# Optimization experiments

Hardware: AMD Instinct MI355X
Metric: run time of the kernel (lower is better)

The kernel has to match this reference:

```python
import jax, jax.numpy as jnp
import numpy as np

B, C, H, W = 256, 512, 14, 14  # C = rnn_size
S = 7                          # spp_size

def setup_inputs() -> dict:
    key = jax.random.key(0)
    ks = jax.random.split(key, 8)
    sd = 1.0 / np.sqrt(C)
    return {
        "att_v": jax.random.normal(ks[0], (B, C, H, W), dtype=jnp.float32),
        "h": jax.random.normal(ks[1], (B, C), dtype=jnp.float32),
        # a2a: Linear(rnn_size, rnn_size)
        "Wa": jax.random.uniform(ks[2], (C, C), jnp.float32, -sd, sd),
        "ba": jax.random.uniform(ks[3], (C,), jnp.float32, -sd, sd),
        # h2a: Linear(rnn_size, rnn_size)
        "Wh": jax.random.uniform(ks[4], (C, C), jnp.float32, -sd, sd),
        "bh": jax.random.uniform(ks[5], (C,), jnp.float32, -sd, sd),
        # d2d: Linear(rnn_size, 1)
        "Wd": jax.random.uniform(ks[6], (C,), jnp.float32, -sd, sd),
        "bd": jax.random.uniform(ks[7], (1,), jnp.float32, -sd, sd),
    }

def reference(att_v, h, Wa, ba, Wh, bh, Wd, bd):
    b, c, hh, ww = att_v.shape
    # AdaptiveAvgPool2d(S) with H,W divisible by S -> block mean
    pooled = att_v.reshape(b, c, S, hh // S, S, ww // S).mean(axis=(3, 5))  # [B,C,S,S]
    a = pooled.reshape(b, c, S * S).transpose(0, 2, 1)  # [B, N=49, C]
    av = jnp.einsum('bnc,dc->bnd', a, Wa) + ba          # a2a, torch Linear: x @ W.T + b
    ah = h @ Wh.T + bh                                  # h2a, [B,C]
    dot = jnp.tanh(av + ah[:, None, :])                 # broadcast add + tanh
    scores = jnp.einsum('bnd,d->bn', dot, Wd) + bd[0]   # d2d -> [B, N]
    weight = jax.nn.softmax(scores, axis=-1)            # over attention positions
    att_res = jnp.einsum('bnc,bn->bc', a, weight)       # bmm(att^T, weight)
    return att_res
```

## Files before the change

kernel.cpp:

```cpp
#include <hip/hip_runtime.h>
#include <hip/hip_bf16.h>

#define BATCH 256
#define CDIM  512
#define NPOS  49
#define MROWS 12544
#define ASTRIDE 520

typedef __attribute__((ext_vector_type(8))) short bf16x8_t;
typedef __attribute__((ext_vector_type(4))) float f32x4_t;

#define WS_NEED 15081472u

__device__ __forceinline__ void load_lds16(const void* g, void* l) {
    __builtin_amdgcn_global_load_lds(
        (const __attribute__((address_space(1))) void*)g,
        (__attribute__((address_space(3))) void*)l, 16, 0, 0);
}

__global__ __launch_bounds__(256) void prep(
    const float* __restrict__ Wa, const float* __restrict__ Wh,
    const float* __restrict__ h,
    __hip_bfloat16* __restrict__ Wab, __hip_bfloat16* __restrict__ Whb,
    __hip_bfloat16* __restrict__ hb) {
    int gid = blockIdx.x * 256 + threadIdx.x;
    const float* src; __hip_bfloat16* dst; int idx;
    if (gid < 65536)       { src = Wa; dst = Wab; idx = gid; }
    else if (gid < 131072) { src = Wh; dst = Whb; idx = gid - 65536; }
    else                   { src = h;  dst = hb;  idx = gid - 131072; }
    float4 v = ((const float4*)src)[idx];
    dst[idx * 4 + 0] = __float2bfloat16(v.x);
    dst[idx * 4 + 1] = __float2bfloat16(v.y);
    dst[idx * 4 + 2] = __float2bfloat16(v.z);
    dst[idx * 4 + 3] = __float2bfloat16(v.w);
}

__global__ __launch_bounds__(256, 6) void pool_kernel(
    const float* __restrict__ att_v, __hip_bfloat16* __restrict__ pooled) {
    __shared__ float4 lds[32 * 49];
    const int b  = blockIdx.x >> 4;
    const int cg = blockIdx.x & 15;
    const int t  = threadIdx.x;

    const float4* src = (const float4*)(att_v + ((size_t)b * CDIM + cg * 32) * 196);
    #pragma unroll
    for (int k = 0; k < 7; ++k) {
        int idx = t + k * 256;
        if (idx < 1568) lds[idx] = src[idx];
    }
    __syncthreads();

    const int i = t >> 5;
    const int c = t & 31;
    if (i < 7) {
        const float4* fp = &lds[c * 49 + 7 * i];
        float4 f0 = fp[0], f1 = fp[1], f2 = fp[2], f3 = fp[3];
        float4 f4 = fp[4], f5 = fp[5], f6 = fp[6];
        float p[7];
        p[0] = f0.x + f0.y + f3.z + f3.w;
        p[1] = f0.z + f0.w + f4.x + f4.y;
        p[2] = f1.x + f1.y + f4.z + f4.w;
        p[3] = f1.z + f1.w + f5.x + f5.y;
        p[4] = f2.x + f2.y + f5.z + f5.w;
        p[5] = f2.z + f2.w + f6.x + f6.y;
        p[6] = f3.x + f3.y + f6.z + f6.w;
        __hip_bfloat16* outp = pooled + ((size_t)b * NPOS + i * 7) * CDIM + cg * 32 + c;
        #pragma unroll
        for (int j = 0; j < 7; ++j)
            outp[(size_t)j * CDIM] = __float2bfloat16(p[j] * 0.25f);
    }
}

__global__ __launch_bounds__(256, 4) void ah_gemm(
    const __hip_bfloat16* __restrict__ A,
    const __hip_bfloat16* __restrict__ Bw,
    const float* __restrict__ ba, const float* __restrict__ bh,
    float* __restrict__ ahb) {
    __shared__ __hip_bfloat16 aT[64 * 32];
    __shared__ __hip_bfloat16 bT[64 * 32];
    const int mt = blockIdx.x & 3;
    const int nt = blockIdx.x >> 2;
    const int t = threadIdx.x;
    const int wave = t >> 6, lane = t & 63;
    const int wm = wave & 1, wn = wave >> 1;
    const int q = lane >> 4, r = lane & 15;
    const int m0 = mt * 64, n0 = nt * 64;

    const __hip_bfloat16* Ag = A + (size_t)(m0 + (t >> 2)) * CDIM + (t & 3) * 8;
    const __hip_bfloat16* Bg = Bw + (size_t)(n0 + (t >> 2)) * CDIM + (t & 3) * 8;
    char* aD = (char*)aT + t * 16;
    char* bD = (char*)bT + t * 16;

    f32x4_t acc[2][2];
    #pragma unroll
    for (int rt = 0; rt < 2; ++rt)
        #pragma unroll
        for (int ct = 0; ct < 2; ++ct) acc[rt][ct] = (f32x4_t){0.f, 0.f, 0.f, 0.f};

    for (int ks = 0; ks < 16; ++ks) {
        load_lds16(Ag + ks * 32, aD);
        load_lds16(Bg + ks * 32, bD);
        __syncthreads();
        bf16x8_t af[2], bf[2];
        #pragma unroll
        for (int rt = 0; rt < 2; ++rt)
            af[rt] = *(const bf16x8_t*)&aT[(wm * 32 + rt * 16 + r) * 32 + q * 8];
        #pragma unroll
        for (int ct = 0; ct < 2; ++ct)
            bf[ct] = *(const bf16x8_t*)&bT[(wn * 32 + ct * 16 + r) * 32 + q * 8];
        #pragma unroll
        for (int rt = 0; rt < 2; ++rt)
            #pragma unroll
            for (int ct = 0; ct < 2; ++ct)
                acc[rt][ct] = __builtin_amdgcn_mfma_f32_16x16x32_bf16(
                    af[rt], bf[ct], acc[rt][ct], 0, 0, 0);
        __syncthreads();
    }
    #pragma unroll
    for (int ct = 0; ct < 2; ++ct) {
        const int col = n0 + wn * 32 + ct * 16 + r;
        const float bias = ba[col] + bh[col];
        #pragma unroll
        for (int rt = 0; rt < 2; ++rt)
            #pragma unroll
            for (int rg = 0; rg < 4; ++rg) {
                const int row = m0 + wm * 32 + rt * 16 + q * 4 + rg;
                ahb[(size_t)row * CDIM + col] = acc[rt][ct][rg] + bias;
            }
    }
}

__global__ __launch_bounds__(256, 4) void gemm_score3(
    const __hip_bfloat16* __restrict__ A,
    const __hip_bfloat16* __restrict__ Bw,
    const float* __restrict__ ahb,
    const float* __restrict__ Wd,
    float* __restrict__ scores8) {
    __shared__ __hip_bfloat16 aT[64 * 32];
    __shared__ __hip_bfloat16 bT[128 * 32];
    const int b  = blockIdx.x >> 2;
    const int nt = blockIdx.x & 3;
    const int t = threadIdx.x;
    const int wave = t >> 6, lane = t & 63;
    const int wm = wave & 1, wn = wave >> 1;
    const int q = lane >> 4, r = lane & 15;
    const int m0 = b * NPOS;
    const int n0 = nt * 128;

    const __hip_bfloat16* Ag = A + (size_t)(m0 + (t >> 2)) * CDIM + (t & 3) * 8;
    const __hip_bfloat16* Bg = Bw + (size_t)(n0 + (t >> 2)) * CDIM + (t & 3) * 8;
    char* aD = (char*)aT + t * 16;
    char* bD = (char*)bT + t * 16;

    f32x4_t acc[2][4];
    #pragma unroll
    for (int rt = 0; rt < 2; ++rt)
        #pragma unroll
        for (int ct = 0; ct < 4; ++ct) acc[rt][ct] = (f32x4_t){0.f, 0.f, 0.f, 0.f};

    for (int ks = 0; ks < 16; ++ks) {
        load_lds16(Ag + ks * 32, aD);
        load_lds16(Bg + ks * 32, bD);
        load_lds16(Bg + (size_t)64 * CDIM + ks * 32, bD + 4096);
        __syncthreads();
        bf16x8_t af[2], bf[4];
        #pragma unroll
        for (int rt = 0; rt < 2; ++rt)
            af[rt] = *(const bf16x8_t*)&aT[(wm * 32 + rt * 16 + r) * 32 + q * 8];
        #pragma unroll
        for (int ct = 0; ct < 4; ++ct)
            bf[ct] = *(const bf16x8_t*)&bT[(wn * 64 + ct * 16 + r) * 32 + q * 8];
        #pragma unroll
        for (int rt = 0; rt < 2; ++rt)
            #pragma unroll
            for (int ct = 0; ct < 4; ++ct)
                acc[rt][ct] = __builtin_amdgcn_mfma_f32_16x16x32_bf16(
                    af[rt], bf[ct], acc[rt][ct], 0, 0, 0);
        __syncthreads();
    }

    float rsum[2][4];
    #pragma unroll
    for (int rt = 0; rt < 2; ++rt)
        #pragma unroll
        for (int rg = 0; rg < 4; ++rg) rsum[rt][rg] = 0.f;

    const float* ahp = ahb + (size_t)b * CDIM;
    #pragma unroll
    for (int ct = 0; ct < 4; ++ct) {
        const int col = n0 + wn * 64 + ct * 16 + r;
        const float ah = ahp[col];
        const float wd = Wd[col];
        #pragma unroll
        for (int rt = 0; rt < 2; ++rt)
            #pragma unroll
            for (int rg = 0; rg < 4; ++rg) {
                float x = acc[rt][ct][rg] + ah;
                float e = __expf(2.f * x);
                rsum[rt][rg] += (1.f - 2.f / (e + 1.f)) * wd;
            }
    }
    #pragma unroll
    for (int m = 1; m < 16; m <<= 1)
        #pragma unroll
        for (int rt = 0; rt < 2; ++rt)
            #pragma unroll
            for (int rg = 0; rg < 4; ++rg)
                rsum[rt][rg] += __shfl_xor(rsum[rt][rg], m, 64);
    if (r == 0) {
        float* seg = scores8 + (size_t)(nt * 2 + wn) * MROWS + m0;
        #pragma unroll
        for (int rt = 0; rt < 2; ++rt)
            #pragma unroll
            for (int rg = 0; rg < 4; ++rg) {
                const int row = wm * 32 + rt * 16 + q * 4 + rg;
                if (row < NPOS) seg[row] = rsum[rt][rg];
            }
    }
}

__global__ __launch_bounds__(256) void softmax_wsum(
    const float* __restrict__ scores8, const __hip_bfloat16* __restrict__ pooled,
    float* __restrict__ out) {
    __shared__ float s_lds[NPOS];
    const int b  = blockIdx.x >> 1;
    const int ch = (blockIdx.x & 1) * 256 + threadIdx.x;
    if (threadIdx.x < NPOS) {
        float s = 0.f;
        #pragma unroll
        for (int seg = 0; seg < 8; ++seg)
            s += scores8[(size_t)seg * MROWS + b * NPOS + threadIdx.x];
        s_lds[threadIdx.x] = s;
    }
    __syncthreads();
    float vmax = -3.0e38f;
    #pragma unroll
    for (int n = 0; n < NPOS; ++n) vmax = fmaxf(vmax, s_lds[n]);
    const __hip_bfloat16* Ap = pooled + (size_t)b * NPOS * CDIM + ch;
    float sum = 0.f, accv = 0.f;
    #pragma unroll
    for (int n = 0; n < NPOS; ++n) {
        float e = __expf(s_lds[n] - vmax);
        sum += e;
        accv += e * __bfloat162float(Ap[(size_t)n * CDIM]);
    }
    out[b * CDIM + ch] = accv / sum;
}

__global__ void prep_convert(const float* __restrict__ Wa,
                             const float* __restrict__ Wh,
                             __hip_bfloat16* __restrict__ Wab,
                             __hip_bfloat16* __restrict__ Whb) {
    int gid = blockIdx.x * blockDim.x + threadIdx.x;
    const int quarter = (CDIM * CDIM) / 4;
    const float4* src; __hip_bfloat16* dst; int idx;
    if (gid < quarter) { src = (const float4*)Wa; dst = Wab; idx = gid; }
    else               { src = (const float4*)Wh; dst = Whb; idx = gid - quarter; }
    float4 v = src[idx];
    dst[idx * 4 + 0] = __float2bfloat16(v.x);
    dst[idx * 4 + 1] = __float2bfloat16(v.y);
    dst[idx * 4 + 2] = __float2bfloat16(v.z);
    dst[idx * 4 + 3] = __float2bfloat16(v.w);
}

__global__ __launch_bounds__(512, 2) void att_spp_main(
    const float* __restrict__ att_v, const float* __restrict__ h,
    const float* __restrict__ ba, const float* __restrict__ bh,
    const float* __restrict__ Wd,
    const __hip_bfloat16* __restrict__ Wab, const __hip_bfloat16* __restrict__ Whb,
    float* __restrict__ out) {
    __shared__ __hip_bfloat16 a_lds[64 * ASTRIDE];
    __shared__ __hip_bfloat16 h_lds[CDIM];
    __shared__ float babh_lds[CDIM];
    __shared__ float wd_lds[CDIM];
    __shared__ float scores_lds[64];
    __shared__ float weights_lds[NPOS];
    const int b = blockIdx.x, t = threadIdx.x;
    h_lds[t]    = __float2bfloat16(h[b * CDIM + t]);
    babh_lds[t] = ba[t] + bh[t];
    wd_lds[t]   = Wd[t];
    if (t < 64) scores_lds[t] = 0.f;
    for (int idx = t; idx < (64 - NPOS) * ASTRIDE; idx += 512)
        a_lds[NPOS * ASTRIDE + idx] = __float2bfloat16(0.f);
    {
        const int jj = t & 7, g = t >> 3;
        const float2* att2 = (const float2*)(att_v + (size_t)b * CDIM * 196);
        if (jj < 7) {
            for (int ci = 0; ci < 8; ++ci) {
                const int c = g + (ci << 6), cbase = c * 98;
                #pragma unroll
                for (int i = 0; i < 7; ++i) {
                    float2 v0 = att2[cbase + i * 14 + jj];
                    float2 v1 = att2[cbase + i * 14 + 7 + jj];
                    a_lds[(i * 7 + jj) * ASTRIDE + c] =
                        __float2bfloat16((v0.x + v0.y + v1.x + v1.y) * 0.25f);
                }
            }
        }
    }
    __syncthreads();
    const int wave = t >> 6, lane = t & 63, q = lane >> 4, r = lane & 15;
    f32x4_t acc[4][4];
    #pragma unroll
    for (int rt = 0; rt < 4; ++rt)
        #pragma unroll
        for (int ct = 0; ct < 4; ++ct) acc[rt][ct] = (f32x4_t){0.f,0.f,0.f,0.f};
    const int dBase = wave * 64 + r;
    for (int ks = 0; ks < 16; ++ks) {
        const int k0 = ks * 32 + q * 8;
        bf16x8_t af[4], bf[4];
        #pragma unroll
        for (int rt = 0; rt < 4; ++rt)
            af[rt] = *(const bf16x8_t*)&a_lds[(rt * 16 + r) * ASTRIDE + k0];
        #pragma unroll
        for (int ct = 0; ct < 4; ++ct)
            bf[ct] = *(const bf16x8_t*)&Wab[(size_t)(dBase + ct * 16) * CDIM + k0];
        #pragma unroll
        for (int rt = 0; rt < 4; ++rt)
            #pragma unroll
            for (int ct = 0; ct < 4; ++ct)
                acc[rt][ct] = __builtin_amdgcn_mfma_f32_16x16x32_bf16(
                    af[rt], bf[ct], acc[rt][ct], 0, 0, 0);
    }
    for (int ks = 0; ks < 16; ++ks) {
        const int k0 = ks * 32 + q * 8;
        bf16x8_t af = *(const bf16x8_t*)&h_lds[k0];
        bf16x8_t bf[4];
        #pragma unroll
        for (int ct = 0; ct < 4; ++ct)
            bf[ct] = *(const bf16x8_t*)&Whb[(size_t)(dBase + ct * 16) * CDIM + k0];
        #pragma unroll
        for (int rt = 0; rt < 4; ++rt)
            #pragma unroll
            for (int ct = 0; ct < 4; ++ct)
                acc[rt][ct] = __builtin_amdgcn_mfma_f32_16x16x32_bf16(
                    af, bf[ct], acc[rt][ct], 0, 0, 0);
    }
    float part[4][4];
    #pragma unroll
    for (int rt = 0; rt < 4; ++rt)
        #pragma unroll
        for (int rg = 0; rg < 4; ++rg) part[rt][rg] = 0.f;
    #pragma unroll
    for (int ct = 0; ct < 4; ++ct) {
        const int d = dBase + ct * 16;
        const float bias = babh_lds[d], wd = wd_lds[d];
        #pragma unroll
        for (int rt = 0; rt < 4; ++rt)
            #pragma unroll
            for (int rg = 0; rg < 4; ++rg) {
                float x = acc[rt][ct][rg] + bias;
                float e = __expf(2.f * x);
                part[rt][rg] += (1.f - 2.f / (e + 1.f)) * wd;
            }
    }
    #pragma unroll
    for (int m = 1; m < 16; m <<= 1)
        #pragma unroll
        for (int rt = 0; rt < 4; ++rt)
            #pragma unroll
            for (int rg = 0; rg < 4; ++rg)
                part[rt][rg] += __shfl_xor(part[rt][rg], m, 64);
    if (r == 0) {
        #pragma unroll
        for (int rt = 0; rt < 4; ++rt)
            #pragma unroll
            for (int rg = 0; rg < 4; ++rg)
                atomicAdd(&scores_lds[rt * 16 + q * 4 + rg], part[rt][rg]);
    }
    __syncthreads();
    if (wave == 0) {
        float v = (lane < NPOS) ? scores_lds[lane] : -3.0e38f;
        float vmax = v;
        #pragma unroll
        for (int m = 1; m < 64; m <<= 1) vmax = fmaxf(vmax, __shfl_xor(vmax, m, 64));
        float e = (lane < NPOS) ? __expf(v - vmax) : 0.f;
        float s = e;
        #pragma unroll
        for (int m = 1; m < 64; m <<= 1) s += __shfl_xor(s, m, 64);
        if (lane < NPOS) weights_lds[lane] = e / s;
    }
    __syncthreads();
    float sum = 0.f;
    #pragma unroll
    for (int n = 0; n < NPOS; ++n)
        sum += __bfloat162float(a_lds[n * ASTRIDE + t]) * weights_lds[n];
    out[b * CDIM + t] = sum;
}

extern "C" void kernel_launch(void* const* d_in, const int* in_sizes, int n_in,
                              void* d_out, int out_size, void* d_ws, size_t ws_size,
                              hipStream_t stream) {
    const float* att_v = (const float*)d_in[0];
    const float* h     = (const float*)d_in[1];
    const float* Wa    = (const float*)d_in[2];
    const float* ba    = (const float*)d_in[3];
    const float* Wh    = (const float*)d_in[4];
    const float* bh    = (const float*)d_in[5];
    const float* Wd    = (const float*)d_in[6];

    if (ws_size >= WS_NEED) {
        char* ws = (char*)d_ws;
        __hip_bfloat16* Wab     = (__hip_bfloat16*)(ws);
        __hip_bfloat16* Whb     = (__hip_bfloat16*)(ws + 524288);
        __hip_bfloat16* hb      = (__hip_bfloat16*)(ws + 1048576);
        __hip_bfloat16* pooled  = (__hip_bfloat16*)(ws + 1310720);
        float*          ahb     = (float*)(ws + 14155776);
        float*          scores8 = (float*)(ws + 14680064);

        prep<<<640, 256, 0, stream>>>(Wa, Wh, h, Wab, Whb, hb);
        pool_kernel<<<4096, 256, 0, stream>>>(att_v, pooled);
        ah_gemm<<<32, 256, 0, stream>>>(hb, Whb, ba, bh, ahb);
        gemm_score3<<<1024, 256, 0, stream>>>(pooled, Wab, ahb, Wd, scores8);
        softmax_wsum<<<512, 256, 0, stream>>>(scores8, pooled, (float*)d_out);
    } else {
        __hip_bfloat16* Wab = (__hip_bfloat16*)d_ws;
        __hip_bfloat16* Whb = Wab + (size_t)CDIM * CDIM;
        prep_convert<<<512, 256, 0, stream>>>(Wa, Wh, Wab, Whb);
        att_spp_main<<<BATCH, 512, 0, stream>>>(att_v, h, ba, bh, Wd, Wab, Whb,
                                                (float*)d_out);
    }
}
```

Baseline: 198.8 us.

## Fuse pool, weight prep and h2a GEMV into one kernel; deepen K step

Merges the prep, pooling and ah_gemm launches into a single kernel whose block ranges handle pooling, Wa bf16 conversion and an fp32 h2a GEMV per batch. This drops two launches and the Wh/h bf16 conversion. The score GEMM now loads 64-wide K slices per barrier, halving the number of sync rounds at the cost of double the LDS. The h2a path becomes a scalar fp32 GEMV with strided Wh row reads, which may be slow and uncoalesced.

```diff
diff --git a/kernel.cpp b/kernel.cpp
--- a/kernel.cpp
+++ b/kernel.cpp
@@ -10,7 +10,7 @@
 typedef __attribute__((ext_vector_type(8))) short bf16x8_t;
 typedef __attribute__((ext_vector_type(4))) float f32x4_t;
 
-#define WS_NEED 15081472u
+#define WS_NEED 14295040u
 
 __device__ __forceinline__ void load_lds16(const void* g, void* l) {
     __builtin_amdgcn_global_load_lds(
@@ -18,126 +18,85 @@
         (__attribute__((address_space(3))) void*)l, 16, 0, 0);
 }
 
-__global__ __launch_bounds__(256) void prep(
-    const float* __restrict__ Wa, const float* __restrict__ Wh,
+__global__ __launch_bounds__(256, 6) void k1_pool_prep_ah(
+    const float* __restrict__ att_v,
     const float* __restrict__ h,
-    __hip_bfloat16* __restrict__ Wab, __hip_bfloat16* __restrict__ Whb,
-    __hip_bfloat16* __restrict__ hb) {
-    int gid = blockIdx.x * 256 + threadIdx.x;
-    const float* src; __hip_bfloat16* dst; int idx;
-    if (gid < 65536)       { src = Wa; dst = Wab; idx = gid; }
-    else if (gid < 131072) { src = Wh; dst = Whb; idx = gid - 65536; }
-    else                   { src = h;  dst = hb;  idx = gid - 131072; }
-    float4 v = ((const float4*)src)[idx];
-    dst[idx * 4 + 0] = __float2bfloat16(v.x);
-    dst[idx * 4 + 1] = __float2bfloat16(v.y);
-    dst[idx * 4 + 2] = __float2bfloat16(v.z);
-    dst[idx * 4 + 3] = __float2bfloat16(v.w);
-}
-
-__global__ __launch_bounds__(256, 6) void pool_kernel(
-    const float* __restrict__ att_v, __hip_bfloat16* __restrict__ pooled) {
-    __shared__ float4 lds[32 * 49];
-    const int b  = blockIdx.x >> 4;
-    const int cg = blockIdx.x & 15;
-    const int t  = threadIdx.x;
-
-    const float4* src = (const float4*)(att_v + ((size_t)b * CDIM + cg * 32) * 196);
-    #pragma unroll
-    for (int k = 0; k < 7; ++k) {
-        int idx = t + k * 256;
-        if (idx < 1568) lds[idx] = src[idx];
-    }
-    __syncthreads();
-
-    const int i = t >> 5;
-    const int c = t & 31;
-    if (i < 7) {
-        const float4* fp = &lds[c * 49 + 7 * i];
-        float4 f0 = fp[0], f1 = fp[1], f2 = fp[2], f3 = fp[3];
-        float4 f4 = fp[4], f5 = fp[5], f6 = fp[6];
-        float p[7];
-        p[0] = f0.x + f0.y + f3.z + f3.w;
-        p[1] = f0.z + f0.w + f4.x + f4.y;
-        p[2] = f1.x + f1.y + f4.z + f4.w;
-        p[3] = f1.z + f1.w + f5.x + f5.y;
-        p[4] = f2.x + f2.y + f5.z + f5.w;
-        p[5] = f2.z + f2.w + f6.x + f6.y;
-        p[6] = f3.x + f3.y + f6.z + f6.w;
-        __hip_bfloat16* outp = pooled + ((size_t)b * NPOS + i * 7) * CDIM + cg * 32 + c;
-        #pragma unroll
-        for (int j = 0; j < 7; ++j)
-            outp[(size_t)j * CDIM] = __float2bfloat16(p[j] * 0.25f);
-    }
-}
-
-__global__ __launch_bounds__(256, 4) void ah_gemm(
-    const __hip_bfloat16* __restrict__ A,
-    const __hip_bfloat16* __restrict__ Bw,
+    const float* __restrict__ Wa,
+    const float* __restrict__ Wh,
     const float* __restrict__ ba, const float* __restrict__ bh,
+    __hip_bfloat16* __restrict__ pooled,
+    __hip_bfloat16* __restrict__ Wab,
     float* __restrict__ ahb) {
-    __shared__ __hip_bfloat16 aT[64 * 32];
-    __shared__ __hip_bfloat16 bT[64 * 32];
-    const int mt = blockIdx.x & 3;
-    const int nt = blockIdx.x >> 2;
-    const int t = threadIdx.x;
-    const int wave = t >> 6, lane = t & 63;
-    const int wm = wave & 1, wn = wave >> 1;
-    const int q = lane >> 4, r = lane & 15;
-    const int m0 = mt * 64, n0 = nt * 64;
-
-    const __hip_bfloat16* Ag = A + (size_t)(m0 + (t >> 2)) * CDIM + (t & 3) * 8;
-    const __hip_bfloat16* Bg = Bw + (size_t)(n0 + (t >> 2)) * CDIM + (t & 3) * 8;
-    char* aD = (char*)aT + t * 16;
-    char* bD = (char*)bT + t * 16;
-
-    f32x4_t acc[2][2];
-    #pragma unroll
-    for (int rt = 0; rt < 2; ++rt)
-        #pragma unroll
-        for (int ct = 0; ct < 2; ++ct) acc[rt][ct] = (f32x4_t){0.f, 0.f, 0.f, 0.f};
-
-    for (int ks = 0; ks < 16; ++ks) {
-        load_lds16(Ag + ks * 32, aD);
-        load_lds16(Bg + ks * 32, bD);
+    __shared__ float4 lds4[32 * 49];
+    const int bid = blockIdx.x;
+    const int t   = threadIdx.x;
+
+    if (bid < 4096) {
+        const int b  = bid >> 4;
+        const int cg = bid & 15;
+        const float4* src = (const float4*)(att_v + ((size_t)b * CDIM + cg * 32) * 196);
+        #pragma unroll
+        for (int k = 0; k < 7; ++k) {
+            int idx = t + k * 256;
+            if (idx < 1568) lds4[idx] = src[idx];
+        }
         __syncthreads();
-        bf16x8_t af[2], bf[2];
-        #pragma unroll
-        for (int rt = 0; rt < 2; ++rt)
-            af[rt] = *(const bf16x8_t*)&aT[(wm * 32 + rt * 16 + r) * 32 + q * 8];
-        #pragma unroll
-        for (int ct = 0; ct < 2; ++ct)
-            bf[ct] = *(const bf16x8_t*)&bT[(wn * 32 + ct * 16 + r) * 32 + q * 8];
-        #pragma unroll
-        for (int rt = 0; rt < 2; ++rt)
-            #pragma unroll
-            for (int ct = 0; ct < 2; ++ct)
-                acc[rt][ct] = __builtin_amdgcn_mfma_f32_16x16x32_bf16(
-                    af[rt], bf[ct], acc[rt][ct], 0, 0, 0);
+        const int i = t >> 5;
+        const int c = t & 31;
+        if (i < 7) {
+            const float4* fp = &lds4[c * 49 + 7 * i];
+            float4 f0 = fp[0], f1 = fp[1], f2 = fp[2], f3 = fp[3];
+            float4 f4 = fp[4], f5 = fp[5], f6 = fp[6];
+            float p[7];
+            p[0] = f0.x + f0.y + f3.z + f3.w;
+            p[1] = f0.z + f0.w + f4.x + f4.y;
+            p[2] = f1.x + f1.y + f4.z + f4.w;
+            p[3] = f1.z + f1.w + f5.x + f5.y;
+            p[4] = f2.x + f2.y + f5.z + f5.w;
+            p[5] = f2.z + f2.w + f6.x + f6.y;
+            p[6] = f3.x + f3.y + f6.z + f6.w;
+            __hip_bfloat16* outp =
+                pooled + ((size_t)b * NPOS + i * 7) * CDIM + cg * 32 + c;
+            #pragma unroll
+            for (int j = 0; j < 7; ++j)
+                outp[(size_t)j * CDIM] = __float2bfloat16(p[j] * 0.25f);
+        }
+    } else if (bid < 4352) {
+        const int idx = (bid - 4096) * 256 + t;
+        float4 v = ((const float4*)Wa)[idx];
+        Wab[idx * 4 + 0] = __float2bfloat16(v.x);
+        Wab[idx * 4 + 1] = __float2bfloat16(v.y);
+        Wab[idx * 4 + 2] = __float2bfloat16(v.z);
+        Wab[idx * 4 + 3] = __float2bfloat16(v.w);
+    } else {
+        const int b = bid - 4352;
+        float* h_s = (float*)lds4;
+        h_s[t]       = h[b * CDIM + t];
+        h_s[t + 256] = h[b * CDIM + t + 256];
         __syncthreads();
-    }
-    #pragma unroll
-    for (int ct = 0; ct < 2; ++ct) {
-        const int col = n0 + wn * 32 + ct * 16 + r;
-        const float bias = ba[col] + bh[col];
-        #pragma unroll
-        for (int rt = 0; rt < 2; ++rt)
-            #pragma unroll
-            for (int rg = 0; rg < 4; ++rg) {
-                const int row = m0 + wm * 32 + rt * 16 + q * 4 + rg;
-                ahb[(size_t)row * CDIM + col] = acc[rt][ct][rg] + bias;
-            }
-    }
-}
-
-__global__ __launch_bounds__(256, 4) void gemm_score3(
+        const int d0 = t, d1 = t + 256;
+        const float* w0 = Wh + (size_t)d0 * CDIM;
+        const float* w1 = Wh + (size_t)d1 * CDIM;
+        float a0 = 0.f, a1 = 0.f;
+        #pragma unroll 8
+        for (int c = 0; c < CDIM; ++c) {
+            float hc = h_s[c];
+            a0 += hc * w0[c];
+            a1 += hc * w1[c];
+        }
+        ahb[(size_t)b * CDIM + d0] = a0 + ba[d0] + bh[d0];
+        ahb[(size_t)b * CDIM + d1] = a1 + ba[d1] + bh[d1];
+    }
+}
+
+__global__ __launch_bounds__(256, 4) void gemm_score(
     const __hip_bfloat16* __restrict__ A,
     const __hip_bfloat16* __restrict__ Bw,
     const float* __restrict__ ahb,
     const float* __restrict__ Wd,
     float* __restrict__ scores8) {
-    __shared__ __hip_bfloat16 aT[64 * 32];
-    __shared__ __hip_bfloat16 bT[128 * 32];
+    __shared__ __hip_bfloat16 aT[2 * 64 * 32];
+    __shared__ __hip_bfloat16 bT[2 * 128 * 32];
     const int b  = blockIdx.x >> 2;
     const int nt = blockIdx.x & 3;
     const int t = threadIdx.x;
@@ -148,7 +107,8 @@
     const int n0 = nt * 128;
 
     const __hip_bfloat16* Ag = A + (size_t)(m0 + (t >> 2)) * CDIM + (t & 3) * 8;
-    const __hip_bfloat16* Bg = Bw + (size_t)(n0 + (t >> 2)) * CDIM + (t & 3) * 8;
+    const __hip_bfloat16* Bg0 = Bw + (size_t)(n0 + (t >> 2)) * CDIM + (t & 3) * 8;
+    const __hip_bfloat16* Bg1 = Bw + (size_t)(n0 + 64 + (t >> 2)) * CDIM + (t & 3) * 8;
     char* aD = (char*)aT + t * 16;
     char* bD = (char*)bT + t * 16;
 
@@ -158,24 +118,33 @@
         #pragma unroll
         for (int ct = 0; ct < 4; ++ct) acc[rt][ct] = (f32x4_t){0.f, 0.f, 0.f, 0.f};
 
-    for (int ks = 0; ks < 16; ++ks) {
-        load_lds16(Ag + ks * 32, aD);
-        load_lds16(Bg + ks * 32, bD);
-        load_lds16(Bg + (size_t)64 * CDIM + ks * 32, bD + 4096);
+    for (int ks = 0; ks < 8; ++ks) {
+        const int k0 = ks * 64;
+        load_lds16(Ag + k0, aD);
+        load_lds16(Ag + k0 + 32, aD + 4096);
+        load_lds16(Bg0 + k0, bD);
+        load_lds16(Bg1 + k0, bD + 4096);
+        load_lds16(Bg0 + k0 + 32, bD + 8192);
+        load_lds16(Bg1 + k0 + 32, bD + 12288);
         __syncthreads();
-        bf16x8_t af[2], bf[4];
-        #pragma unroll
-        for (int rt = 0; rt < 2; ++rt)
-            af[rt] = *(const bf16x8_t*)&aT[(wm * 32 + rt * 16 + r) * 32 + q * 8];
-        #pragma unroll
-        for (int ct = 0; ct < 4; ++ct)
-            bf[ct] = *(const bf16x8_t*)&bT[(wn * 64 + ct * 16 + r) * 32 + q * 8];
-        #pragma unroll
-        for (int rt = 0; rt < 2; ++rt)
+        #pragma unroll
+        for (int s = 0; s < 2; ++s) {
+            const __hip_bfloat16* aS = aT + s * 2048;
+            const __hip_bfloat16* bS = bT + s * 4096;
+            bf16x8_t af[2], bf[4];
+            #pragma unroll
+            for (int rt = 0; rt < 2; ++rt)
+                af[rt] = *(const bf16x8_t*)&aS[(wm * 32 + rt * 16 + r) * 32 + q * 8];
             #pragma unroll
             for (int ct = 0; ct < 4; ++ct)
-                acc[rt][ct] = __builtin_amdgcn_mfma_f32_16x16x32_bf16(
-                    af[rt], bf[ct], acc[rt][ct], 0, 0, 0);
+                bf[ct] = *(const bf16x8_t*)&bS[(wn * 64 + ct * 16 + r) * 32 + q * 8];
+            #pragma unroll
+            for (int rt = 0; rt < 2; ++rt)
+                #pragma unroll
+                for (int ct = 0; ct < 4; ++ct)
+                    acc[rt][ct] = __builtin_amdgcn_mfma_f32_16x16x32_bf16(
+                        af[rt], bf[ct], acc[rt][ct], 0, 0, 0);
+        }
         __syncthreads();
     }
 
@@ -402,16 +371,13 @@
     if (ws_size >= WS_NEED) {
         char* ws = (char*)d_ws;
         __hip_bfloat16* Wab     = (__hip_bfloat16*)(ws);
-        __hip_bfloat16* Whb     = (__hip_bfloat16*)(ws + 524288);
-        __hip_bfloat16* hb      = (__hip_bfloat16*)(ws + 1048576);
-        __hip_bfloat16* pooled  = (__hip_bfloat16*)(ws + 1310720);
-        float*          ahb     = (float*)(ws + 14155776);
-        float*          scores8 = (float*)(ws + 14680064);
-
-        prep<<<640, 256, 0, stream>>>(Wa, Wh, h, Wab, Whb, hb);
-        pool_kernel<<<4096, 256, 0, stream>>>(att_v, pooled);
-        ah_gemm<<<32, 256, 0, stream>>>(hb, Whb, ba, bh, ahb);
-        gemm_score3<<<1024, 256, 0, stream>>>(pooled, Wab, ahb, Wd, scores8);
+        __hip_bfloat16* pooled  = (__hip_bfloat16*)(ws + 524288);
+        float*          ahb     = (float*)(ws + 13369344);
+        float*          scores8 = (float*)(ws + 13893632);
+
+        k1_pool_prep_ah<<<4608, 256, 0, stream>>>(att_v, h, Wa, Wh, ba, bh,
+                                                  pooled, Wab, ahb);
+        gemm_score<<<1024, 256, 0, stream>>>(pooled, Wab, ahb, Wd, scores8);
         softmax_wsum<<<512, 256, 0, stream>>>(scores8, pooled, (float*)d_out);
     } else {
         __hip_bfloat16* Wab = (__hip_bfloat16*)d_ws;
```

Measured after the change: 299.7 us. +50.8%, slower.
